# Kernel tuning notes

Measured on AMD Instinct MI355X. Metric: run time of the kernel, lower is better.

## Reference

```python
import jax, jax.numpy as jnp
import numpy as np

B, T, C, H = 1, 4096, 768, 12
D = C // H  # 64


def setup_inputs() -> dict:
    key = jax.random.key(0)
    k1, k2, k3, k4, k5 = jax.random.split(key, 5)
    x = jax.random.normal(k1, (B, T, C), dtype=jnp.float32)
    # causal mask: 1.0 where attention is DISALLOWED (strict upper triangle)
    mask = (1.0 - jnp.tril(jnp.ones((T, T), dtype=jnp.float32)))[None, None, :, :]
    s_attn = 1.0 / np.sqrt(C)
    W_qkv = jax.random.normal(k2, (C, 3 * C), dtype=jnp.float32) * s_attn
    b_qkv = jnp.zeros((3 * C,), dtype=jnp.float32)
    W_proj = jax.random.normal(k3, (C, C), dtype=jnp.float32) * s_attn
    b_proj = jnp.zeros((C,), dtype=jnp.float32)
    return {"x": x, "mask": mask, "W_qkv": W_qkv, "b_qkv": b_qkv,
            "W_proj": W_proj, "b_proj": b_proj}


def reference(x, mask, W_qkv, b_qkv, W_proj, b_proj):
    qkv = jnp.einsum('btc,cf->btf', x, W_qkv) + b_qkv        # [B,T,3C]
    q, k, v = jnp.split(qkv, 3, axis=2)
    # [B,T,C] -> [B,H,T,D]
    q = q.reshape(B, T, H, D).transpose(0, 2, 1, 3)
    k = k.reshape(B, T, H, D).transpose(0, 2, 1, 3)
    v = v.reshape(B, T, H, D).transpose(0, 2, 1, 3)
    att = jnp.einsum('bhqd,bhkd->bhqk', q, k) * (1.0 / jnp.sqrt(jnp.float32(D)))
    att = att + mask * (-1e9)
    att = jax.nn.softmax(att, axis=-1)                        # [B,H,T,T]
    y = jnp.einsum('bhqk,bhkd->bhqd', att, v)                 # [B,H,T,D]
    y = y.transpose(0, 2, 1, 3).reshape(B, T, C)
    return jnp.einsum('btc,cf->btf', y, W_proj) + b_proj
```

## Files before the change

kernel.cpp:

```cpp
#include <hip/hip_runtime.h>
#include <hip/hip_bf16.h>

typedef unsigned short u16t;
typedef short bf16x8 __attribute__((ext_vector_type(8)));
typedef short bf16x4 __attribute__((ext_vector_type(4)));
typedef float f32x4 __attribute__((ext_vector_type(4)));

#define T_SEQ 4096
#define NH    12
#define HD    64
#define C3    2304
#define CDIM  768
#define STRIP_KV 512
#define SLOTS 144
#define SC_F  0.18033688011112042f

__device__ __forceinline__ float bf2f(u16t u) {
  union { unsigned int i; float f; } c; c.i = ((unsigned int)u) << 16; return c.f;
}
__device__ __forceinline__ u16t f2bf(float f) {
  union { float f; unsigned int i; } c; c.f = f;
  unsigned int u = c.i;
  u += 0x7fffu + ((u >> 16) & 1u);
  return (u16t)(u >> 16);
}
__device__ __forceinline__ unsigned pk2bf(float a, float b) {
  __hip_bfloat162 h = __float22bfloat162_rn(make_float2(a, b));
  union { __hip_bfloat162 h; unsigned u; } c; c.h = h; return c.u;
}
__device__ __forceinline__ void gload16(const u16t* g, u16t* l) {
  __builtin_amdgcn_global_load_lds((const __attribute__((address_space(1))) void*)g,
                                   (__attribute__((address_space(3))) void*)l,
                                   16, 0, 0);
}

#define BARRIER_LGKM() __asm__ __volatile__("s_waitcnt lgkmcnt(0)\n\ts_barrier" ::: "memory")

__global__ __launch_bounds__(256) void convert_to_bf16(const float* __restrict__ in,
                                                       u16t* __restrict__ out, int n8) {
  int i = blockIdx.x * 256 + threadIdx.x;
  const int stride = gridDim.x * 256;
  for (; i < n8; i += stride) {
    const float4 a = ((const float4*)in)[2 * i];
    const float4 b = ((const float4*)in)[2 * i + 1];
    union { uint4 u; unsigned w[4]; } o;
    o.w[0] = pk2bf(a.x, a.y); o.w[1] = pk2bf(a.z, a.w);
    o.w[2] = pk2bf(b.x, b.y); o.w[3] = pk2bf(b.z, b.w);
    ((uint4*)out)[i] = o.u;
  }
}

__global__ __launch_bounds__(256) void transpose_weights(const float* __restrict__ Wqkv,
                                                         const float* __restrict__ Wproj,
                                                         u16t* __restrict__ WqkvT,
                                                         u16t* __restrict__ WprojT) {
  __shared__ u16t tile[32][33];
  const int z = blockIdx.z;
  const int Cc = z ? CDIM : C3;
  if (z && blockIdx.x >= (unsigned)(CDIM / 32)) return;
  const float* in = z ? Wproj : Wqkv;
  u16t* out = z ? WprojT : WqkvT;
  const int tx = threadIdx.x, ty = threadIdx.y;
  const int c0 = blockIdx.x * 32, r0 = blockIdx.y * 32;
#pragma unroll
  for (int i = 0; i < 32; i += 8)
    tile[ty + i][tx] = f2bf(in[(size_t)(r0 + ty + i) * Cc + c0 + tx]);
  __syncthreads();
#pragma unroll
  for (int i = 0; i < 32; i += 8)
    out[(size_t)(c0 + ty + i) * CDIM + r0 + tx] = tile[tx][ty + i];
}

template <int MT, int NF, bool OUTF32>
__global__ __launch_bounds__(256) void gemm_bt_bias(
    const u16t* __restrict__ A, const u16t* __restrict__ Bt,
    const float* __restrict__ bias, void* __restrict__ Cout,
    int M, int N, int K, int qcols, float qscale) {
  constexpr int BN = 32 * NF;
  constexpr int MI = MT / 32;
  constexpr int LA = MT / 64;
  constexpr int LB = NF / 2;
  constexpr int L  = LA + LB;
  __shared__ u16t lA[3][MT * 32];
  __shared__ u16t lB[3][BN * 32];
  const int t = threadIdx.x;
  const int lane = t & 63;
  const int wid  = t >> 6;
  const int quad = lane >> 4, l16 = lane & 15;

  const int gx = gridDim.x;
  const int nwg = gx * (int)gridDim.y;
  int bid = (int)blockIdx.y * gx + (int)blockIdx.x;
  if ((nwg & 7) == 0) bid = (bid & 7) * (nwg >> 3) + (bid >> 3);
  const int m0 = (bid / gx) * MT, n0 = (bid % gx) * BN;

  const int wm = (wid >> 1) * (16 * MI), wn = (wid & 1) * (16 * NF);
  const int rswz = (quad ^ ((l16 >> 1) & 3)) * 8;

  f32x4 acc[MI][NF];
#pragma unroll
  for (int i = 0; i < MI; ++i)
#pragma unroll
    for (int j = 0; j < NF; ++j) acc[i][j] = (f32x4){0.f, 0.f, 0.f, 0.f};

  auto stage = [&](int b, int k0) {
#pragma unroll
    for (int rd = 0; rd < LA; ++rd) {
      const int e = rd * 256 + t;
      const int row = e >> 2;
      const int ch  = (e & 3) ^ ((row >> 1) & 3);
      gload16(A + (size_t)(m0 + row) * K + k0 + ch * 8, &lA[b][e * 8]);
    }
#pragma unroll
    for (int rd = 0; rd < LB; ++rd) {
      const int e = rd * 256 + t;
      const int row = e >> 2;
      const int ch  = (e & 3) ^ ((row >> 1) & 3);
      gload16(Bt + (size_t)(n0 + row) * K + k0 + ch * 8, &lB[b][e * 8]);
    }
  };
  auto compute = [&](int b) {
    bf16x8 af[MI], bfr[NF];
#pragma unroll
    for (int i = 0; i < MI; ++i)
      af[i] = *(const bf16x8*)&lA[b][(wm + i * 16 + l16) * 32 + rswz];
#pragma unroll
    for (int i = 0; i < NF; ++i)
      bfr[i] = *(const bf16x8*)&lB[b][(wn + i * 16 + l16) * 32 + rswz];
#pragma unroll
    for (int i = 0; i < MI; ++i)
#pragma unroll
      for (int j = 0; j < NF; ++j)
        acc[i][j] = __builtin_amdgcn_mfma_f32_16x16x32_bf16(af[i], bfr[j], acc[i][j], 0, 0, 0);
  };

  const int NT = K >> 5;
  stage(0, 0);
  stage(1, 32);
  for (int tt = 0; tt < NT; ++tt) {
    if (tt < NT - 1) {
      __asm__ __volatile__("s_waitcnt vmcnt(%0)" :: "n"(L) : "memory");
    } else {
      __asm__ __volatile__("s_waitcnt vmcnt(0)" ::: "memory");
    }
    __builtin_amdgcn_s_barrier();
    __builtin_amdgcn_sched_barrier(0);
    compute(tt % 3);
    if (tt + 2 < NT) stage((tt + 2) % 3, (tt + 2) * 32);
  }

#pragma unroll
  for (int j = 0; j < NF; ++j) {
    const int col = n0 + wn + j * 16 + l16;
    const float bv = bias[col];
    const float cs = (col < qcols) ? qscale : 1.0f;
#pragma unroll
    for (int i = 0; i < MI; ++i) {
      const int rowb = m0 + wm + i * 16 + quad * 4;
#pragma unroll
      for (int r = 0; r < 4; ++r) {
        const float val = (acc[i][j][r] + bv) * cs;
        const size_t idx = (size_t)(rowb + r) * N + col;
        if (OUTF32) ((float*)Cout)[idx] = val;
        else        ((u16t*)Cout)[idx] = f2bf(val);
      }
    }
  }
}

#define KSTR 88
#define VSTR 88

__global__ __launch_bounds__(256, 4) void attn_partial(const u16t* __restrict__ qkv,
                                                       u16t* __restrict__ pO,
                                                       float* __restrict__ pL) {
  const int h     = blockIdx.x;
  const int strip = blockIdx.y;
  const int qt    = 31 - (int)blockIdx.z;
  const int q0 = qt * 128;
  const int kv_begin = strip * STRIP_KV;
  const int kv_end   = q0 + 128;
  if (kv_begin >= kv_end) return;
  const int kv_stop = (kv_begin + STRIP_KV < kv_end) ? kv_begin + STRIP_KV : kv_end;
  const int a = qt >> 2, b = qt & 3;
  const int slot = (a + 1) * (2 * a + b) + strip;

  __shared__ u16t lK[64 * KSTR];
  __shared__ u16t lVt[64 * VSTR];

  const int t = threadIdx.x;
  const int lane = t & 63;
  const int wid  = t >> 6;
  const int quad = lane >> 4, l16 = lane & 15;
  const int wr = q0 + wid * 32;

  const int krow = t >> 3, kcol = (t & 7) * 8;
  const int vk0 = 4 * (t >> 4);
  const int vd0 = 4 * (t & 15);
  const int vswz = (t & 3) << 3;
  const u16t* Kbase = qkv + CDIM + h * HD;
  const u16t* Vbase = qkv + 2 * CDIM + h * HD;

  bf16x8 qf[2][2];
#pragma unroll
  for (int qn = 0; qn < 2; ++qn) {
    const int row = wr + qn * 16 + l16;
#pragma unroll
    for (int kd = 0; kd < 2; ++kd)
      qf[qn][kd] = *(const bf16x8*)(qkv + (size_t)row * C3 + h * HD + kd * 32 + quad * 8);
  }

  f32x4 oaccT[4][2];
  f32x4 laccT[2];
#pragma unroll
  for (int dn = 0; dn < 4; ++dn)
#pragma unroll
    for (int qn = 0; qn < 2; ++qn) oaccT[dn][qn] = (f32x4){0.f, 0.f, 0.f, 0.f};
#pragma unroll
  for (int qn = 0; qn < 2; ++qn) laccT[qn] = (f32x4){0.f, 0.f, 0.f, 0.f};
  bf16x4 ones4;
#pragma unroll
  for (int i = 0; i < 4; ++i) ones4[i] = (short)0x3F80;

  const int pswz = ((l16 >> 2) & 3) << 3;

  uint4 kreg0, kreg1;
  union { uint2 u; u16t hw[4]; } vreg[4];

#define LOAD_TILE(KV0)                                                        \
  do {                                                                        \
    kreg0 = *(const uint4*)(Kbase + (size_t)((KV0) + krow) * C3 + kcol);      \
    kreg1 = *(const uint4*)(Kbase + (size_t)((KV0) + krow + 32) * C3 + kcol); \
    _Pragma("unroll")                                                         \
    for (int i = 0; i < 4; ++i)                                               \
      vreg[i].u = *(const uint2*)(Vbase + (size_t)((KV0) + vk0 + i) * C3 + vd0); \
  } while (0)

#define STORE_TILE()                                                          \
  do {                                                                        \
    *(uint4*)&lK[krow * KSTR + kcol] = kreg0;                                 \
    *(uint4*)&lK[(krow + 32) * KSTR + kcol] = kreg1;                          \
    _Pragma("unroll")                                                         \
    for (int j = 0; j < 4; ++j) {                                             \
      union { uint2 u; u16t hw[4]; } w;                                       \
      w.hw[0] = vreg[0].hw[j]; w.hw[1] = vreg[1].hw[j];                       \
      w.hw[2] = vreg[2].hw[j]; w.hw[3] = vreg[3].hw[j];                       \
      *(uint2*)&lVt[(vd0 + j) * VSTR + (vk0 ^ vswz)] = w.u;                   \
    }                                                                         \
  } while (0)

  LOAD_TILE(kv_begin);
  STORE_TILE();

  for (int kv0 = kv_begin; kv0 < kv_stop; kv0 += 64) {
    const bool havenext = (kv0 + 64 < kv_stop);
    if (havenext) LOAD_TILE(kv0 + 64);
    BARRIER_LGKM();

    if (kv0 <= wr + 31) {
      f32x4 sacc[4][2];
#pragma unroll
      for (int kvt = 0; kvt < 4; ++kvt) {
        bf16x8 kf0 = *(const bf16x8*)&lK[(kvt * 16 + l16) * KSTR + quad * 8];
        bf16x8 kf1 = *(const bf16x8*)&lK[(kvt * 16 + l16) * KSTR + 32 + quad * 8];
#pragma unroll
        for (int qn = 0; qn < 2; ++qn) {
          f32x4 s = (f32x4){0.f, 0.f, 0.f, 0.f};
          s = __builtin_amdgcn_mfma_f32_16x16x32_bf16(kf0, qf[qn][0], s, 0, 0, 0);
          s = __builtin_amdgcn_mfma_f32_16x16x32_bf16(kf1, qf[qn][1], s, 0, 0, 0);
          sacc[kvt][qn] = s;
        }
      }
      const bool need_mask = (kv0 + 63 > wr);
      bf16x4 pbf[4][2];
#pragma unroll
      for (int kvt = 0; kvt < 4; ++kvt)
#pragma unroll
        for (int qn = 0; qn < 2; ++qn) {
          const int qg = wr + qn * 16 + l16;
          float pv[4];
#pragma unroll
          for (int r = 0; r < 4; ++r) {
            const int kvg = kv0 + kvt * 16 + quad * 4 + r;
            float p = __builtin_amdgcn_exp2f(sacc[kvt][qn][r]);
            if (need_mask && (kvg > qg)) p = 0.f;
            pv[r] = p;
          }
          union { bf16x4 v; unsigned u[2]; } pw;
          pw.u[0] = pk2bf(pv[0], pv[1]);
          pw.u[1] = pk2bf(pv[2], pv[3]);
          pbf[kvt][qn] = pw.v;
        }
#pragma unroll
      for (int kvt = 0; kvt < 4; ++kvt) {
        const int kvcol = (kvt * 16 + quad * 4) ^ pswz;
#pragma unroll
        for (int qn = 0; qn < 2; ++qn)
          laccT[qn] = __builtin_amdgcn_mfma_f32_16x16x16bf16_1k(
              ones4, pbf[kvt][qn], laccT[qn], 0, 0, 0);
#pragma unroll
        for (int dn = 0; dn < 4; ++dn) {
          bf16x4 vf = *(const bf16x4*)&lVt[(dn * 16 + l16) * VSTR + kvcol];
#pragma unroll
          for (int qn = 0; qn < 2; ++qn)
            oaccT[dn][qn] = __builtin_amdgcn_mfma_f32_16x16x16bf16_1k(
                vf, pbf[kvt][qn], oaccT[dn][qn], 0, 0, 0);
        }
      }
    }
    BARRIER_LGKM();
    if (havenext) STORE_TILE();
  }

  {
    u16t* scr = &lVt[wid * 16 * 80];
    u16t* po = pO + ((size_t)h * SLOTS + slot) * 128 * HD;
    float* pl = pL + ((size_t)h * SLOTS + slot) * 128;
#pragma unroll
    for (int qn = 0; qn < 2; ++qn) {
#pragma unroll
      for (int dn = 0; dn < 4; ++dn) {
        union { bf16x4 v; unsigned u[2]; } w;
        w.u[0] = pk2bf(oaccT[dn][qn][0], oaccT[dn][qn][1]);
        w.u[1] = pk2bf(oaccT[dn][qn][2], oaccT[dn][qn][3]);
        *(bf16x4*)&scr[l16 * 80 + dn * 16 + quad * 4] = w.v;
      }
      __asm__ __volatile__("s_waitcnt lgkmcnt(0)" ::: "memory");
      const int ql = wid * 32 + qn * 16 + l16;
      uint4 w0 = *(const uint4*)&scr[l16 * 80 + quad * 16];
      uint4 w1 = *(const uint4*)&scr[l16 * 80 + quad * 16 + 8];
      u16t* dst = po + (size_t)ql * HD + quad * 16;
      *(uint4*)dst = w0;
      *(uint4*)(dst + 8) = w1;
      if (quad == 0) pl[ql] = laccT[qn][0];
      __asm__ __volatile__("s_waitcnt lgkmcnt(0)" ::: "memory");
    }
  }
#undef LOAD_TILE
#undef STORE_TILE
}

__global__ __launch_bounds__(256) void attn_normalize(const u16t* __restrict__ pO,
                                                      const float* __restrict__ pL,
                                                      u16t* __restrict__ y) {
  const int i = blockIdx.x * 256 + threadIdx.x;
  const int q = i / (CDIM / 8), c8 = (i % (CDIM / 8)) * 8;
  const int h = c8 >> 6, d = c8 & 63;
  const int qt = q >> 7, ql = q & 127;
  const int a = qt >> 2, b = qt & 3;
  const int base = (a + 1) * (2 * a + b);
  const int ns = a + 1;
  float o[8] = {0.f, 0.f, 0.f, 0.f, 0.f, 0.f, 0.f, 0.f};
  float l = 0.f;
  for (int s = 0; s < ns; ++s) {
    const size_t sl = (size_t)h * SLOTS + base + s;
    union { uint4 u; u16t hw[8]; } v;
    v.u = *(const uint4*)&pO[(sl * 128 + ql) * HD + d];
#pragma unroll
    for (int j = 0; j < 8; ++j) o[j] += bf2f(v.hw[j]);
    l += pL[sl * 128 + ql];
  }
  const float rl = 1.0f / l;
  union { uint4 u; unsigned w[4]; } wv;
#pragma unroll
  for (int j = 0; j < 4; ++j)
    wv.w[j] = pk2bf(o[2 * j] * rl, o[2 * j + 1] * rl);
  *(uint4*)&y[(size_t)q * CDIM + c8] = wv.u;
}

extern "C" void kernel_launch(void* const* d_in, const int* in_sizes, int n_in,
                              void* d_out, int out_size, void* d_ws, size_t ws_size,
                              hipStream_t stream) {
  const float* x     = (const float*)d_in[0];
  const float* Wqkv  = (const float*)d_in[2];
  const float* bqkv  = (const float*)d_in[3];
  const float* Wproj = (const float*)d_in[4];
  const float* bproj = (const float*)d_in[5];

  u16t* qkv    = (u16t*)d_ws;
  u16t* ybuf   = qkv    + (size_t)T_SEQ * C3;
  u16t* WqkvT  = ybuf   + (size_t)T_SEQ * CDIM;
  u16t* WprojT = WqkvT  + (size_t)C3 * CDIM;
  u16t* pO     = WprojT + (size_t)CDIM * CDIM;
  float* pL    = (float*)(pO + (size_t)NH * SLOTS * 128 * HD);

  convert_to_bf16<<<1536, 256, 0, stream>>>(x, ybuf, T_SEQ * CDIM / 8);
  transpose_weights<<<dim3(C3 / 32, CDIM / 32, 2), dim3(32, 8), 0, stream>>>(
      Wqkv, Wproj, WqkvT, WprojT);
  gemm_bt_bias<128, 4, false><<<dim3(C3 / 128, T_SEQ / 128), 256, 0, stream>>>(
      ybuf, WqkvT, bqkv, qkv, T_SEQ, C3, CDIM, CDIM, SC_F);
  attn_partial<<<dim3(NH, 8, T_SEQ / 128), 256, 0, stream>>>(qkv, pO, pL);
  attn_normalize<<<(T_SEQ * CDIM / 8) / 256, 256, 0, stream>>>(pO, pL, ybuf);
  gemm_bt_bias<128, 2, true><<<dim3(CDIM / 64, T_SEQ / 128), 256, 0, stream>>>(
      ybuf, WprojT, bproj, d_out, T_SEQ, CDIM, CDIM, 0, 1.0f);
}
```

Measured before the change: 218.2 us.

## Double-buffer K/V LDS tiles in attention, fuse prep kernels, add setprio

The attention kernel now keeps two LDS buffers for K and V^T. The next tile is stored into the alternate buffer right after compute, which leaves one barrier per iteration instead of two. MFMA sections are wrapped in s_setprio to favour compute waves. The bf16 conversion of x and the weight transpose are merged into one launch via a third grid z-slice, removing one kernel launch. The cost is double the LDS per block (about 45KB), which may lower occupancy under the launch bound of 4 blocks.

```diff
diff --git a/kernel.cpp b/kernel.cpp
--- a/kernel.cpp
+++ b/kernel.cpp
@@ -36,31 +36,33 @@
 
 #define BARRIER_LGKM() __asm__ __volatile__("s_waitcnt lgkmcnt(0)\n\ts_barrier" ::: "memory")
 
-__global__ __launch_bounds__(256) void convert_to_bf16(const float* __restrict__ in,
-                                                       u16t* __restrict__ out, int n8) {
-  int i = blockIdx.x * 256 + threadIdx.x;
-  const int stride = gridDim.x * 256;
-  for (; i < n8; i += stride) {
-    const float4 a = ((const float4*)in)[2 * i];
-    const float4 b = ((const float4*)in)[2 * i + 1];
-    union { uint4 u; unsigned w[4]; } o;
-    o.w[0] = pk2bf(a.x, a.y); o.w[1] = pk2bf(a.z, a.w);
-    o.w[2] = pk2bf(b.x, b.y); o.w[3] = pk2bf(b.z, b.w);
-    ((uint4*)out)[i] = o.u;
-  }
-}
-
-__global__ __launch_bounds__(256) void transpose_weights(const float* __restrict__ Wqkv,
-                                                         const float* __restrict__ Wproj,
-                                                         u16t* __restrict__ WqkvT,
-                                                         u16t* __restrict__ WprojT) {
+__global__ __launch_bounds__(256) void prep_inputs(const float* __restrict__ x,
+                                                   const float* __restrict__ Wqkv,
+                                                   const float* __restrict__ Wproj,
+                                                   u16t* __restrict__ xbf,
+                                                   u16t* __restrict__ WqkvT,
+                                                   u16t* __restrict__ WprojT) {
+  const int z = blockIdx.z;
+  const int tx = threadIdx.x, ty = threadIdx.y;
+  if (z == 2) {
+    const int t = ty * 32 + tx;
+    const int n8 = T_SEQ * CDIM / 8;
+    const int i = ((int)blockIdx.y * (int)gridDim.x + (int)blockIdx.x) * 256 + t;
+    if (i < n8) {
+      const float4 a = ((const float4*)x)[2 * i];
+      const float4 b = ((const float4*)x)[2 * i + 1];
+      union { uint4 u; unsigned w[4]; } o;
+      o.w[0] = pk2bf(a.x, a.y); o.w[1] = pk2bf(a.z, a.w);
+      o.w[2] = pk2bf(b.x, b.y); o.w[3] = pk2bf(b.z, b.w);
+      ((uint4*)xbf)[i] = o.u;
+    }
+    return;
+  }
   __shared__ u16t tile[32][33];
-  const int z = blockIdx.z;
   const int Cc = z ? CDIM : C3;
   if (z && blockIdx.x >= (unsigned)(CDIM / 32)) return;
   const float* in = z ? Wproj : Wqkv;
   u16t* out = z ? WprojT : WqkvT;
-  const int tx = threadIdx.x, ty = threadIdx.y;
   const int c0 = blockIdx.x * 32, r0 = blockIdx.y * 32;
 #pragma unroll
   for (int i = 0; i < 32; i += 8)
@@ -185,8 +187,8 @@
   const int a = qt >> 2, b = qt & 3;
   const int slot = (a + 1) * (2 * a + b) + strip;
 
-  __shared__ u16t lK[64 * KSTR];
-  __shared__ u16t lVt[64 * VSTR];
+  __shared__ u16t lK[2][64 * KSTR];
+  __shared__ u16t lVt[2][64 * VSTR];
 
   const int t = threadIdx.x;
   const int lane = t & 63;
@@ -236,33 +238,38 @@
       vreg[i].u = *(const uint2*)(Vbase + (size_t)((KV0) + vk0 + i) * C3 + vd0); \
   } while (0)
 
-#define STORE_TILE()                                                          \
+#define STORE_TILE(BUF)                                                       \
   do {                                                                        \
-    *(uint4*)&lK[krow * KSTR + kcol] = kreg0;                                 \
-    *(uint4*)&lK[(krow + 32) * KSTR + kcol] = kreg1;                          \
+    *(uint4*)&lK[BUF][krow * KSTR + kcol] = kreg0;                            \
+    *(uint4*)&lK[BUF][(krow + 32) * KSTR + kcol] = kreg1;                     \
     _Pragma("unroll")                                                         \
     for (int j = 0; j < 4; ++j) {                                             \
       union { uint2 u; u16t hw[4]; } w;                                       \
       w.hw[0] = vreg[0].hw[j]; w.hw[1] = vreg[1].hw[j];                       \
       w.hw[2] = vreg[2].hw[j]; w.hw[3] = vreg[3].hw[j];                       \
-      *(uint2*)&lVt[(vd0 + j) * VSTR + (vk0 ^ vswz)] = w.u;                   \
+      *(uint2*)&lVt[BUF][(vd0 + j) * VSTR + (vk0 ^ vswz)] = w.u;              \
     }                                                                         \
   } while (0)
 
+  const int nt = (kv_stop - kv_begin) >> 6;
+
   LOAD_TILE(kv_begin);
-  STORE_TILE();
-
-  for (int kv0 = kv_begin; kv0 < kv_stop; kv0 += 64) {
-    const bool havenext = (kv0 + 64 < kv_stop);
+  STORE_TILE(0);
+  BARRIER_LGKM();
+
+  for (int i = 0; i < nt; ++i) {
+    const int kv0 = kv_begin + i * 64;
+    const bool havenext = (i + 1 < nt);
     if (havenext) LOAD_TILE(kv0 + 64);
-    BARRIER_LGKM();
+    const int bsel = i & 1;
 
     if (kv0 <= wr + 31) {
+      __builtin_amdgcn_s_setprio(1);
       f32x4 sacc[4][2];
 #pragma unroll
       for (int kvt = 0; kvt < 4; ++kvt) {
-        bf16x8 kf0 = *(const bf16x8*)&lK[(kvt * 16 + l16) * KSTR + quad * 8];
-        bf16x8 kf1 = *(const bf16x8*)&lK[(kvt * 16 + l16) * KSTR + 32 + quad * 8];
+        bf16x8 kf0 = *(const bf16x8*)&lK[bsel][(kvt * 16 + l16) * KSTR + quad * 8];
+        bf16x8 kf1 = *(const bf16x8*)&lK[bsel][(kvt * 16 + l16) * KSTR + 32 + quad * 8];
 #pragma unroll
         for (int qn = 0; qn < 2; ++qn) {
           f32x4 s = (f32x4){0.f, 0.f, 0.f, 0.f};
@@ -300,20 +307,21 @@
               ones4, pbf[kvt][qn], laccT[qn], 0, 0, 0);
 #pragma unroll
         for (int dn = 0; dn < 4; ++dn) {
-          bf16x4 vf = *(const bf16x4*)&lVt[(dn * 16 + l16) * VSTR + kvcol];
+          bf16x4 vf = *(const bf16x4*)&lVt[bsel][(dn * 16 + l16) * VSTR + kvcol];
 #pragma unroll
           for (int qn = 0; qn < 2; ++qn)
             oaccT[dn][qn] = __builtin_amdgcn_mfma_f32_16x16x16bf16_1k(
                 vf, pbf[kvt][qn], oaccT[dn][qn], 0, 0, 0);
         }
       }
-    }
+      __builtin_amdgcn_s_setprio(0);
+    }
+    if (havenext) STORE_TILE(bsel ^ 1);
     BARRIER_LGKM();
-    if (havenext) STORE_TILE();
   }
 
   {
-    u16t* scr = &lVt[wid * 16 * 80];
+    u16t* scr = &lVt[0][wid * 16 * 80];
     u16t* po = pO + ((size_t)h * SLOTS + slot) * 128 * HD;
     float* pl = pL + ((size_t)h * SLOTS + slot) * 128;
 #pragma unroll
@@ -384,9 +392,8 @@
   u16t* pO     = WprojT + (size_t)CDIM * CDIM;
   float* pL    = (float*)(pO + (size_t)NH * SLOTS * 128 * HD);
 
-  convert_to_bf16<<<1536, 256, 0, stream>>>(x, ybuf, T_SEQ * CDIM / 8);
-  transpose_weights<<<dim3(C3 / 32, CDIM / 32, 2), dim3(32, 8), 0, stream>>>(
-      Wqkv, Wproj, WqkvT, WprojT);
+  prep_inputs<<<dim3(C3 / 32, CDIM / 32, 3), dim3(32, 8), 0, stream>>>(
+      x, Wqkv, Wproj, ybuf, WqkvT, WprojT);
   gemm_bt_bias<128, 4, false><<<dim3(C3 / 128, T_SEQ / 128), 256, 0, stream>>>(
       ybuf, WqkvT, bqkv, qkv, T_SEQ, C3, CDIM, CDIM, SC_F);
   attn_partial<<<dim3(NH, 8, T_SEQ / 128), 256, 0, stream>>>(qkv, pO, pL);
```

After: 239.0 us. +9.5%, slower.
